# Kernel optimization log

Measured on AMD Instinct MI355X. Metric: run time of the kernel, lower is better.

Reference implementation:

```python
import jax, jax.numpy as jnp
import numpy as np

N = 500000
D = 128
S = 4096


def setup_inputs() -> dict:
    key = jax.random.key(0)
    ks = jax.random.split(key, 8)
    x = jax.random.normal(ks[0], (N, D), dtype=jnp.float32)
    subnet_id = jax.random.randint(ks[1], (N,), 0, S, dtype=jnp.int32)
    # MLP params (Linear(D,D) x2), LayerNorm params
    lim = 1.0 / np.sqrt(D)
    W1 = jax.random.uniform(ks[2], (D, D), minval=-lim, maxval=lim, dtype=jnp.float32)
    b1 = jax.random.uniform(ks[3], (D,), minval=-lim, maxval=lim, dtype=jnp.float32)
    W2 = jax.random.uniform(ks[4], (D, D), minval=-lim, maxval=lim, dtype=jnp.float32)
    b2 = jax.random.uniform(ks[5], (D,), minval=-lim, maxval=lim, dtype=jnp.float32)
    gamma = jnp.ones((D,), dtype=jnp.float32)
    beta = jnp.zeros((D,), dtype=jnp.float32)
    return {"x": x, "subnet_id": subnet_id, "num_subnets": S,
            "W1": W1, "b1": b1, "W2": W2, "b2": b2, "gamma": gamma, "beta": beta}


def reference(x, subnet_id, num_subnets, W1, b1, W2, b2, gamma, beta):
    # scatter-mean over subnets: [S, D]
    seg_sum = jax.ops.segment_sum(x, subnet_id, num_segments=num_subnets)
    cnt = jax.ops.segment_sum(jnp.ones((x.shape[0],), x.dtype), subnet_id,
                              num_segments=num_subnets)
    mean = seg_sum / jnp.maximum(cnt, 1.0)[:, None]
    # MLP (dropout is identity in eval)
    h = jax.nn.relu(mean @ W1 + b1) @ W2 + b2
    # gather back + residual
    out = x + h[subnet_id]
    # LayerNorm (eps=1e-5)
    mu = jnp.mean(out, axis=-1, keepdims=True)
    var = jnp.var(out, axis=-1, keepdims=True)
    return (out - mu) * jax.lax.rsqrt(var + 1e-5) * gamma + beta
```

## Files before the change

kernel.cpp:

```cpp
#include <hip/hip_runtime.h>
#include <hip/hip_bf16.h>

#define DD  128
#define SS  4096
#define CAP 256

__global__ void scatter_kernel(const int* __restrict__ sid,
                               int* __restrict__ fill,
                               int* __restrict__ idx, int n) {
    const int i4 = blockIdx.x * blockDim.x + threadIdx.x;
    const int n4 = n >> 2;
    if (i4 < n4) {
        int4 v = reinterpret_cast<const int4*>(sid)[i4];
        const int base = i4 * 4;
        int p;
        p = atomicAdd(&fill[v.x], 1); if (p < CAP) idx[v.x * CAP + p] = base;
        p = atomicAdd(&fill[v.y], 1); if (p < CAP) idx[v.y * CAP + p] = base + 1;
        p = atomicAdd(&fill[v.z], 1); if (p < CAP) idx[v.z * CAP + p] = base + 2;
        p = atomicAdd(&fill[v.w], 1); if (p < CAP) idx[v.w * CAP + p] = base + 3;
    }
    const int tail0 = n4 * 4;
    const int ti = tail0 + i4;
    if (ti < n && i4 < (n - tail0)) {
        int id = sid[ti];
        int p = atomicAdd(&fill[id], 1);
        if (p < CAP) idx[id * CAP + p] = ti;
    }
}

__global__ __launch_bounds__(256) void seg_mlp_kernel(
        const float* __restrict__ x,
        const int* __restrict__ idx,
        const int* __restrict__ cnt,
        const float* __restrict__ W1,
        const float* __restrict__ b1,
        const float* __restrict__ W2,
        const float* __restrict__ b2,
        float* __restrict__ h) {
    const int s    = blockIdx.x;
    const int t    = threadIdx.x;
    const int wave = t >> 6;
    const int lane = t & 63;
    const int half = lane >> 5;
    const int sub  = lane & 31;

    __shared__ int    lidx[CAP];
    __shared__ float4 part4[8][32];
    __shared__ float  m[DD];
    __shared__ float  tmp[2][DD];

    const int c  = cnt[s];
    const int cc = (c < CAP) ? c : CAP;

    if (t < cc) lidx[t] = idx[s * CAP + t];
    __syncthreads();

    const int slot = wave * 2 + half;
    float4 acc = make_float4(0.f, 0.f, 0.f, 0.f);
    for (int j = slot; j < cc; j += 8) {
        const int row = lidx[j];
        float4 v = reinterpret_cast<const float4*>(x + (size_t)row * DD)[sub];
        acc.x += v.x; acc.y += v.y; acc.z += v.z; acc.w += v.w;
    }
    part4[slot][sub] = acc;
    __syncthreads();

    if (t < DD) {
        const float* pf = (const float*)part4;
        float sum = 0.f;
#pragma unroll
        for (int p = 0; p < 8; ++p) sum += pf[p * DD + t];
        m[t] = sum / fmaxf((float)c, 1.0f);
    }
    __syncthreads();

    {
        const int col = t & 127, kh = t >> 7, k0 = kh * 64;
        float a = 0.f;
        for (int k = k0; k < k0 + 64; ++k) a = fmaf(m[k], W1[k * DD + col], a);
        tmp[kh][col] = a;
    }
    __syncthreads();
    if (t < DD) m[t] = fmaxf(tmp[0][t] + tmp[1][t] + b1[t], 0.f);
    __syncthreads();

    {
        const int col = t & 127, kh = t >> 7, k0 = kh * 64;
        float a = 0.f;
        for (int k = k0; k < k0 + 64; ++k) a = fmaf(m[k], W2[k * DD + col], a);
        tmp[kh][col] = a;
    }
    __syncthreads();
    if (t < DD) h[(size_t)s * DD + t] = tmp[0][t] + tmp[1][t] + b2[t];
}

__global__ __launch_bounds__(256) void ln_kernel(
        const float* __restrict__ x,
        const int* __restrict__ sid,
        const float* __restrict__ h,
        const float* __restrict__ gamma,
        const float* __restrict__ beta,
        float* __restrict__ out,
        int n) {
    const int wave   = (blockIdx.x * blockDim.x + threadIdx.x) >> 6;
    const int lane   = threadIdx.x & 63;
    const int rrow   = lane >> 4;
    const int rsub   = lane & 15;
    const int nwaves = (gridDim.x * blockDim.x) >> 6;

    const float4* g4 = (const float4*)gamma;
    const float4* b4 = (const float4*)beta;
    const float4 ga = g4[rsub * 2],     ba = b4[rsub * 2];
    const float4 gb = g4[rsub * 2 + 1], bb = b4[rsub * 2 + 1];

    const int ngrp = n >> 2;
    for (int grp = wave; grp < ngrp; grp += nwaves) {
        const int row = grp * 4 + rrow;
        const int id  = sid[row];
        const float4* xr = (const float4*)(x + (size_t)row * DD);
        const float4* hr = (const float4*)(h + (size_t)id * DD);
        float4 o0 = xr[rsub * 2], o1 = xr[rsub * 2 + 1];
        float4 h0 = hr[rsub * 2], h1 = hr[rsub * 2 + 1];
        o0.x += h0.x; o0.y += h0.y; o0.z += h0.z; o0.w += h0.w;
        o1.x += h1.x; o1.y += h1.y; o1.z += h1.z; o1.w += h1.w;

        float sum = ((o0.x + o0.y) + (o0.z + o0.w)) +
                    ((o1.x + o1.y) + (o1.z + o1.w));
        float sq = o0.x * o0.x;
        sq = fmaf(o0.y, o0.y, sq); sq = fmaf(o0.z, o0.z, sq);
        sq = fmaf(o0.w, o0.w, sq); sq = fmaf(o1.x, o1.x, sq);
        sq = fmaf(o1.y, o1.y, sq); sq = fmaf(o1.z, o1.z, sq);
        sq = fmaf(o1.w, o1.w, sq);
#pragma unroll
        for (int off = 8; off; off >>= 1) {
            sum += __shfl_xor(sum, off);
            sq  += __shfl_xor(sq, off);
        }
        const float mu   = sum * (1.0f / DD);
        const float var  = sq * (1.0f / DD) - mu * mu;
        const float rstd = rsqrtf(var + 1e-5f);

        float4 r0, r1;
        r0.x = (o0.x - mu) * rstd * ga.x + ba.x;
        r0.y = (o0.y - mu) * rstd * ga.y + ba.y;
        r0.z = (o0.z - mu) * rstd * ga.z + ba.z;
        r0.w = (o0.w - mu) * rstd * ga.w + ba.w;
        r1.x = (o1.x - mu) * rstd * gb.x + bb.x;
        r1.y = (o1.y - mu) * rstd * gb.y + bb.y;
        r1.z = (o1.z - mu) * rstd * gb.z + bb.z;
        r1.w = (o1.w - mu) * rstd * gb.w + bb.w;
        float4* orow = (float4*)(out + (size_t)row * DD);
        orow[rsub * 2]     = r0;
        orow[rsub * 2 + 1] = r1;
    }
}

extern "C" void kernel_launch(void* const* d_in, const int* in_sizes, int n_in,
                              void* d_out, int out_size, void* d_ws, size_t ws_size,
                              hipStream_t stream) {
    const float* x     = (const float*)d_in[0];
    const int*   sid   = (const int*)d_in[1];
    const float* W1    = (const float*)d_in[3];
    const float* b1    = (const float*)d_in[4];
    const float* W2    = (const float*)d_in[5];
    const float* b2    = (const float*)d_in[6];
    const float* gamma = (const float*)d_in[7];
    const float* beta  = (const float*)d_in[8];
    float*       out   = (float*)d_out;

    const int n = in_sizes[1];

    float* h    = (float*)d_ws;
    int*   fill = (int*)(h + (size_t)SS * DD);
    int*   idx  = fill + SS;

    hipMemsetAsync(fill, 0, SS * sizeof(int), stream);

    const int n4blocks = ((n >> 2) + 255) / 256 + 1;
    scatter_kernel<<<n4blocks, 256, 0, stream>>>(sid, fill, idx, n);
    seg_mlp_kernel<<<SS, 256, 0, stream>>>(x, idx, fill, W1, b1, W2, b2, h);
    ln_kernel<<<2048, 256, 0, stream>>>(x, sid, h, gamma, beta, out, n);
}
```

Before: 245.1 us.

## Fuse memset, scatter, segment MLP and layernorm into one cooperative kernel

Replaces the memset and three separate kernel launches with a single cooperative persistent kernel that uses grid-wide syncs between phases. The segment-mean/MLP phase is reorganized so that each wave handles one subnet: it runs a serial row loop with float2 loads and computes all 128 output columns per wave, where before a 256-thread block served each subnet. The aim is to remove launch and inter-kernel gaps. The trade-offs are grid.sync overhead, fixed 1024-block persistence (the reduction now has 4096 segments over 4096 waves), and less parallelism per segment in the gather loop.

```diff
diff --git a/kernel.cpp b/kernel.cpp
--- a/kernel.cpp
+++ b/kernel.cpp
@@ -1,157 +1,159 @@
 #include <hip/hip_runtime.h>
 #include <hip/hip_bf16.h>
+#include <hip/hip_cooperative_groups.h>
 
-#define DD  128
-#define SS  4096
-#define CAP 256
+namespace cg = cooperative_groups;
 
-__global__ void scatter_kernel(const int* __restrict__ sid,
-                               int* __restrict__ fill,
-                               int* __restrict__ idx, int n) {
-    const int i4 = blockIdx.x * blockDim.x + threadIdx.x;
-    const int n4 = n >> 2;
-    if (i4 < n4) {
-        int4 v = reinterpret_cast<const int4*>(sid)[i4];
-        const int base = i4 * 4;
-        int p;
-        p = atomicAdd(&fill[v.x], 1); if (p < CAP) idx[v.x * CAP + p] = base;
-        p = atomicAdd(&fill[v.y], 1); if (p < CAP) idx[v.y * CAP + p] = base + 1;
-        p = atomicAdd(&fill[v.z], 1); if (p < CAP) idx[v.z * CAP + p] = base + 2;
-        p = atomicAdd(&fill[v.w], 1); if (p < CAP) idx[v.w * CAP + p] = base + 3;
-    }
-    const int tail0 = n4 * 4;
-    const int ti = tail0 + i4;
-    if (ti < n && i4 < (n - tail0)) {
-        int id = sid[ti];
-        int p = atomicAdd(&fill[id], 1);
-        if (p < CAP) idx[id * CAP + p] = ti;
-    }
-}
+#define DD   128
+#define SS   4096
+#define CAP  256
+#define NBLK 1024
+#define NTHR 256
 
-__global__ __launch_bounds__(256) void seg_mlp_kernel(
+__global__ __launch_bounds__(NTHR, 4) void fused_kernel(
         const float* __restrict__ x,
-        const int* __restrict__ idx,
-        const int* __restrict__ cnt,
+        const int*   __restrict__ sid,
         const float* __restrict__ W1,
         const float* __restrict__ b1,
         const float* __restrict__ W2,
         const float* __restrict__ b2,
-        float* __restrict__ h) {
-    const int s    = blockIdx.x;
-    const int t    = threadIdx.x;
-    const int wave = t >> 6;
-    const int lane = t & 63;
-    const int half = lane >> 5;
-    const int sub  = lane & 31;
+        const float* __restrict__ gamma,
+        const float* __restrict__ beta,
+        float*       __restrict__ out,
+        float*       __restrict__ h,
+        int*         __restrict__ fill,
+        int*         __restrict__ idx,
+        int n) {
+    cg::grid_group grid = cg::this_grid();
+    const int t        = threadIdx.x;
+    const int gtid     = blockIdx.x * NTHR + t;
+    const int nthreads = NBLK * NTHR;
 
-    __shared__ int    lidx[CAP];
-    __shared__ float4 part4[8][32];
-    __shared__ float  m[DD];
-    __shared__ float  tmp[2][DD];
-
-    const int c  = cnt[s];
-    const int cc = (c < CAP) ? c : CAP;
-
-    if (t < cc) lidx[t] = idx[s * CAP + t];
-    __syncthreads();
-
-    const int slot = wave * 2 + half;
-    float4 acc = make_float4(0.f, 0.f, 0.f, 0.f);
-    for (int j = slot; j < cc; j += 8) {
-        const int row = lidx[j];
-        float4 v = reinterpret_cast<const float4*>(x + (size_t)row * DD)[sub];
-        acc.x += v.x; acc.y += v.y; acc.z += v.z; acc.w += v.w;
-    }
-    part4[slot][sub] = acc;
-    __syncthreads();
-
-    if (t < DD) {
-        const float* pf = (const float*)part4;
-        float sum = 0.f;
-#pragma unroll
-        for (int p = 0; p < 8; ++p) sum += pf[p * DD + t];
-        m[t] = sum / fmaxf((float)c, 1.0f);
-    }
-    __syncthreads();
+    for (int i = gtid; i < SS; i += nthreads) fill[i] = 0;
+    grid.sync();
 
     {
-        const int col = t & 127, kh = t >> 7, k0 = kh * 64;
-        float a = 0.f;
-        for (int k = k0; k < k0 + 64; ++k) a = fmaf(m[k], W1[k * DD + col], a);
-        tmp[kh][col] = a;
+        const int n4 = n >> 2;
+        for (int i4 = gtid; i4 < n4; i4 += nthreads) {
+            int4 v = reinterpret_cast<const int4*>(sid)[i4];
+            const int base = i4 * 4;
+            int p;
+            p = atomicAdd(&fill[v.x], 1); if (p < CAP) idx[v.x * CAP + p] = base;
+            p = atomicAdd(&fill[v.y], 1); if (p < CAP) idx[v.y * CAP + p] = base + 1;
+            p = atomicAdd(&fill[v.z], 1); if (p < CAP) idx[v.z * CAP + p] = base + 2;
+            p = atomicAdd(&fill[v.w], 1); if (p < CAP) idx[v.w * CAP + p] = base + 3;
+        }
+        const int tail0 = n4 * 4;
+        const int rem   = n - tail0;
+        if (gtid < rem) {
+            int ti = tail0 + gtid;
+            int id = sid[ti];
+            int p  = atomicAdd(&fill[id], 1);
+            if (p < CAP) idx[id * CAP + p] = ti;
+        }
     }
-    __syncthreads();
-    if (t < DD) m[t] = fmaxf(tmp[0][t] + tmp[1][t] + b1[t], 0.f);
-    __syncthreads();
+    grid.sync();
 
     {
-        const int col = t & 127, kh = t >> 7, k0 = kh * 64;
-        float a = 0.f;
-        for (int k = k0; k < k0 + 64; ++k) a = fmaf(m[k], W2[k * DD + col], a);
-        tmp[kh][col] = a;
+        __shared__ int   lidx[4][CAP];
+        __shared__ float mw[4][DD];
+        const int wave = t >> 6;
+        const int lane = t & 63;
+        const int s    = blockIdx.x * 4 + wave;
+
+        const int c  = fill[s];
+        const int cc = (c < CAP) ? c : CAP;
+
+        for (int j = lane; j < cc; j += 64) lidx[wave][j] = idx[s * CAP + j];
+        __syncthreads();
+
+        const float2* x2 = reinterpret_cast<const float2*>(x);
+        float2 acc = make_float2(0.f, 0.f);
+        for (int j = 0; j < cc; ++j) {
+            const int row = lidx[wave][j];
+            float2 v = x2[(size_t)row * 64 + lane];
+            acc.x += v.x;
+            acc.y += v.y;
+        }
+        const float inv = 1.0f / fmaxf((float)c, 1.0f);
+        mw[wave][2 * lane]     = acc.x * inv;
+        mw[wave][2 * lane + 1] = acc.y * inv;
+        __syncthreads();
+
+        float a0 = 0.f, a1 = 0.f;
+        for (int k = 0; k < DD; ++k) {
+            const float mk = mw[wave][k];
+            a0 = fmaf(mk, W1[k * DD + lane], a0);
+            a1 = fmaf(mk, W1[k * DD + lane + 64], a1);
+        }
+        __syncthreads();
+        mw[wave][lane]      = fmaxf(a0 + b1[lane], 0.f);
+        mw[wave][lane + 64] = fmaxf(a1 + b1[lane + 64], 0.f);
+        __syncthreads();
+
+        a0 = 0.f; a1 = 0.f;
+        for (int k = 0; k < DD; ++k) {
+            const float mk = mw[wave][k];
+            a0 = fmaf(mk, W2[k * DD + lane], a0);
+            a1 = fmaf(mk, W2[k * DD + lane + 64], a1);
+        }
+        h[(size_t)s * DD + lane]      = a0 + b2[lane];
+        h[(size_t)s * DD + lane + 64] = a1 + b2[lane + 64];
     }
-    __syncthreads();
-    if (t < DD) h[(size_t)s * DD + t] = tmp[0][t] + tmp[1][t] + b2[t];
-}
+    grid.sync();
 
-__global__ __launch_bounds__(256) void ln_kernel(
-        const float* __restrict__ x,
-        const int* __restrict__ sid,
-        const float* __restrict__ h,
-        const float* __restrict__ gamma,
-        const float* __restrict__ beta,
-        float* __restrict__ out,
-        int n) {
-    const int wave   = (blockIdx.x * blockDim.x + threadIdx.x) >> 6;
-    const int lane   = threadIdx.x & 63;
-    const int rrow   = lane >> 4;
-    const int rsub   = lane & 15;
-    const int nwaves = (gridDim.x * blockDim.x) >> 6;
+    {
+        const int wave   = gtid >> 6;
+        const int lane   = t & 63;
+        const int rrow   = lane >> 4;
+        const int rsub   = lane & 15;
+        const int nwaves = nthreads >> 6;
 
-    const float4* g4 = (const float4*)gamma;
-    const float4* b4 = (const float4*)beta;
-    const float4 ga = g4[rsub * 2],     ba = b4[rsub * 2];
-    const float4 gb = g4[rsub * 2 + 1], bb = b4[rsub * 2 + 1];
+        const float4* g4 = (const float4*)gamma;
+        const float4* b4 = (const float4*)beta;
+        const float4 ga = g4[rsub * 2],     ba = b4[rsub * 2];
+        const float4 gb = g4[rsub * 2 + 1], bb = b4[rsub * 2 + 1];
 
-    const int ngrp = n >> 2;
-    for (int grp = wave; grp < ngrp; grp += nwaves) {
-        const int row = grp * 4 + rrow;
-        const int id  = sid[row];
-        const float4* xr = (const float4*)(x + (size_t)row * DD);
-        const float4* hr = (const float4*)(h + (size_t)id * DD);
-        float4 o0 = xr[rsub * 2], o1 = xr[rsub * 2 + 1];
-        float4 h0 = hr[rsub * 2], h1 = hr[rsub * 2 + 1];
-        o0.x += h0.x; o0.y += h0.y; o0.z += h0.z; o0.w += h0.w;
-        o1.x += h1.x; o1.y += h1.y; o1.z += h1.z; o1.w += h1.w;
+        const int ngrp = n >> 2;
+        for (int grp = wave; grp < ngrp; grp += nwaves) {
+            const int row = grp * 4 + rrow;
+            const int id  = sid[row];
+            const float4* xr = (const float4*)(x + (size_t)row * DD);
+            const float4* hr = (const float4*)(h + (size_t)id * DD);
+            float4 o0 = xr[rsub * 2], o1 = xr[rsub * 2 + 1];
+            float4 h0 = hr[rsub * 2], h1 = hr[rsub * 2 + 1];
+            o0.x += h0.x; o0.y += h0.y; o0.z += h0.z; o0.w += h0.w;
+            o1.x += h1.x; o1.y += h1.y; o1.z += h1.z; o1.w += h1.w;
 
-        float sum = ((o0.x + o0.y) + (o0.z + o0.w)) +
-                    ((o1.x + o1.y) + (o1.z + o1.w));
-        float sq = o0.x * o0.x;
-        sq = fmaf(o0.y, o0.y, sq); sq = fmaf(o0.z, o0.z, sq);
-        sq = fmaf(o0.w, o0.w, sq); sq = fmaf(o1.x, o1.x, sq);
-        sq = fmaf(o1.y, o1.y, sq); sq = fmaf(o1.z, o1.z, sq);
-        sq = fmaf(o1.w, o1.w, sq);
+            float sum = ((o0.x + o0.y) + (o0.z + o0.w)) +
+                        ((o1.x + o1.y) + (o1.z + o1.w));
+            float sq = o0.x * o0.x;
+            sq = fmaf(o0.y, o0.y, sq); sq = fmaf(o0.z, o0.z, sq);
+            sq = fmaf(o0.w, o0.w, sq); sq = fmaf(o1.x, o1.x, sq);
+            sq = fmaf(o1.y, o1.y, sq); sq = fmaf(o1.z, o1.z, sq);
+            sq = fmaf(o1.w, o1.w, sq);
 #pragma unroll
-        for (int off = 8; off; off >>= 1) {
-            sum += __shfl_xor(sum, off);
-            sq  += __shfl_xor(sq, off);
+            for (int off = 8; off; off >>= 1) {
+                sum += __shfl_xor(sum, off);
+                sq  += __shfl_xor(sq, off);
+            }
+            const float mu   = sum * (1.0f / DD);
+            const float var  = sq * (1.0f / DD) - mu * mu;
+            const float rstd = rsqrtf(var + 1e-5f);
+
+            float4 r0, r1;
+            r0.x = (o0.x - mu) * rstd * ga.x + ba.x;
+            r0.y = (o0.y - mu) * rstd * ga.y + ba.y;
+            r0.z = (o0.z - mu) * rstd * ga.z + ba.z;
+            r0.w = (o0.w - mu) * rstd * ga.w + ba.w;
+            r1.x = (o1.x - mu) * rstd * gb.x + bb.x;
+            r1.y = (o1.y - mu) * rstd * gb.y + bb.y;
+            r1.z = (o1.z - mu) * rstd * gb.z + bb.z;
+            r1.w = (o1.w - mu) * rstd * gb.w + bb.w;
+            float4* orow = (float4*)(out + (size_t)row * DD);
+            orow[rsub * 2]     = r0;
+            orow[rsub * 2 + 1] = r1;
         }
-        const float mu   = sum * (1.0f / DD);
-        const float var  = sq * (1.0f / DD) - mu * mu;
-        const float rstd = rsqrtf(var + 1e-5f);
-
-        float4 r0, r1;
-        r0.x = (o0.x - mu) * rstd * ga.x + ba.x;
-        r0.y = (o0.y - mu) * rstd * ga.y + ba.y;
-        r0.z = (o0.z - mu) * rstd * ga.z + ba.z;
-        r0.w = (o0.w - mu) * rstd * ga.w + ba.w;
-        r1.x = (o1.x - mu) * rstd * gb.x + bb.x;
-        r1.y = (o1.y - mu) * rstd * gb.y + bb.y;
-        r1.z = (o1.z - mu) * rstd * gb.z + bb.z;
-        r1.w = (o1.w - mu) * rstd * gb.w + bb.w;
-        float4* orow = (float4*)(out + (size_t)row * DD);
-        orow[rsub * 2]     = r0;
-        orow[rsub * 2 + 1] = r1;
     }
 }
 
@@ -168,16 +170,16 @@
     const float* beta  = (const float*)d_in[8];
     float*       out   = (float*)d_out;
 
-    const int n = in_sizes[1];
+    int n = in_sizes[1];
 
     float* h    = (float*)d_ws;
     int*   fill = (int*)(h + (size_t)SS * DD);
     int*   idx  = fill + SS;
 
-    hipMemsetAsync(fill, 0, SS * sizeof(int), stream);
-
-    const int n4blocks = ((n >> 2) + 255) / 256 + 1;
-    scatter_kernel<<<n4blocks, 256, 0, stream>>>(sid, fill, idx, n);
-    seg_mlp_kernel<<<SS, 256, 0, stream>>>(x, idx, fill, W1, b1, W2, b2, h);
-    ln_kernel<<<2048, 256, 0, stream>>>(x, sid, h, gamma, beta, out, n);
+    void* args[] = { (void*)&x, (void*)&sid, (void*)&W1, (void*)&b1,
+                     (void*)&W2, (void*)&b2, (void*)&gamma, (void*)&beta,
+                     (void*)&out, (void*)&h, (void*)&fill, (void*)&idx,
+                     (void*)&n };
+    hipLaunchCooperativeKernel((const void*)fused_kernel,
+                               dim3(NBLK), dim3(NTHR), args, 0, stream);
 }
```

New measurement: 512.1 us. +108.9%, slower.
